# Kernel tuning notes

Measured on AMD Instinct MI355X. Metric: run time of the kernel, lower is better.

The kernel has to match this reference:

```python
import jax, jax.numpy as jnp
import numpy as np
from jax import lax

G = 4  # feature groups in Group_Linear / adjacency
PAD1, PAD2 = 4, 3  # (kern-1)//2 for kern 9 and 7 ('same' time padding)


def _norm_adj(adj):
    # adj: [G, N, N]; add self-loops then symmetric degree normalization
    N = adj.shape[-1]
    adj = adj + jnp.eye(N, dtype=adj.dtype)
    d = jnp.clip(jnp.sum(adj, axis=-1), 1.0, None) ** -0.5
    return d[..., :, None] * adj * d[..., None, :]


def _gcn(x, adj, W, b):
    # DenseGCNConv2d: x [B,C,N,F], adj [G,N,N], W [G,Cout,Cin], b [Cout]
    B, C, N, F = x.shape
    a = _norm_adj(adj)
    xg = x.reshape(B, C, N, G, F // G).transpose(0, 1, 3, 2, 4)  # [B,C,G,N,Fg]
    h = jnp.einsum('goc,bcgnf->bognf', W, xg)                    # grouped 1x1 conv
    out = jnp.einsum('gnm,bogmf->bognf', a, h)                   # adjacency matmul
    Cout = W.shape[1]
    out = out.transpose(0, 1, 3, 2, 4).reshape(B, Cout, N, F)    # regroup features
    return out + b[None, :, None, None]


def _tpool(x, adj, tw, tb, rp, pad):
    # Dense_TimeDiffPool2d: conv over node dim. x [B,C,N,F] -> [B,N,C,F] as NCHW,
    # kernel tw [N', N, 1, k] as OIHW.
    xt = x.transpose(0, 2, 1, 3)
    out = lax.conv_general_dilated(xt, tw, (1, 1), [(0, 0), (pad, pad)],
                                   dimension_numbers=('NCHW', 'OIHW', 'NCHW'))
    out = out + tb[None, :, None, None]
    out = out.transpose(0, 2, 1, 3)                              # [B,C,N',F]
    s = jnp.einsum('pnik,kj->pn', tw, rp)                        # [N',N] assignment
    out_adj = jnp.einsum('pn,gnm,qm->gpq', s, adj, s)            # pooled adjacency
    return out, out_adj


def _forward(x, adj, W1, b1, tw1, tb1, rp1, W2, b2, tw2, tb2, rp2, Wout, bout):
    h = _gcn(x, adj, W1, b1)
    h, a = _tpool(h, adj, tw1, tb1, rp1, PAD1)
    h = jax.nn.relu(h)
    h = _gcn(h, a, W2, b2)
    h, a = _tpool(h, a, tw2, tb2, rp2, PAD2)
    h = jax.nn.relu(h)
    feat = jnp.mean(h, axis=(-1, -2))                            # global pool [B,C]
    return feat @ Wout.T + bout


def setup_inputs():
    key = jax.random.key(0)
    ks = jax.random.split(key, 10)
    B, Cin, Chid, N, F = 16, 1, 32, 128, 512
    N1, N2 = 64, 32
    k1, k2 = 9, 7
    num_classes = 10
    return {
        'x':    jax.random.normal(ks[0], (B, Cin, N, F), jnp.float32),
        'adj':  jax.random.uniform(ks[1], (G, N, N), jnp.float32),
        'W1':   jax.random.normal(ks[2], (G, Chid, Cin), jnp.float32) * 0.5,
        'b1':   jnp.zeros((Chid,), jnp.float32),
        'tw1':  jax.random.normal(ks[3], (N1, N, 1, k1), jnp.float32) * (1.0 / np.sqrt(N * k1)),
        'tb1':  jnp.zeros((N1,), jnp.float32),
        'rp1':  jax.random.normal(ks[4], (k1, 1), jnp.float32),
        'W2':   jax.random.normal(ks[5], (G, Chid, Chid), jnp.float32) * (1.0 / np.sqrt(Chid)),
        'b2':   jnp.zeros((Chid,), jnp.float32),
        'tw2':  jax.random.normal(ks[6], (N2, N1, 1, k2), jnp.float32) * (1.0 / np.sqrt(N1 * k2)),
        'tb2':  jnp.zeros((N2,), jnp.float32),
        'rp2':  jax.random.normal(ks[7], (k2, 1), jnp.float32),
        'Wout': jax.random.normal(ks[8], (num_classes, Chid), jnp.float32) * (1.0 / np.sqrt(Chid)),
        'bout': jnp.zeros((num_classes,), jnp.float32),
    }


def reference(x, adj, W1, b1, tw1, tb1, rp1, W2, b2, tw2, tb2, rp2, Wout, bout):
    return _forward(x, adj, W1, b1, tw1, tb1, rp1, W2, b2, tw2, tb2, rp2, Wout, bout)
```

## Files before the change

### kernel.cpp

```cpp
#include <hip/hip_runtime.h>
#include <math.h>

#define OFF_D1   0
#define OFF_S1   512
#define OFF_T1   8704
#define OFF_TWB  9280
#define OFF_T    16448
#define OFF_A2   49216
#define OFF_A2H  65600
#define OFF_A2L  73792
#define OFF_PART 81984
#define OFF_AN1  82496
#define OFF_C1H  148032
#define OFF_C1L  295488
#define OFF_XTH  442944
#define OFF_XTL  967232
#define OFF_A    1491520
#define OFF_B    9880128
#define OFF_Z    18268736

typedef short bf16x8 __attribute__((ext_vector_type(8)));
typedef short short4v __attribute__((ext_vector_type(4)));
typedef float f32x4 __attribute__((ext_vector_type(4)));

static __device__ __forceinline__ unsigned short f2bf(float x) {
  union { float f; unsigned u; } v; v.f = x;
  unsigned r = v.u + 0x7FFF + ((v.u >> 16) & 1);
  return (unsigned short)(r >> 16);
}
static __device__ __forceinline__ float bf2f(unsigned short h) {
  union { unsigned u; float f; } v; v.u = ((unsigned)h) << 16;
  return v.f;
}

__global__ __launch_bounds__(256) void prep1_kernel(const float* __restrict__ adj,
    const float* __restrict__ tw1, const float* __restrict__ rp1,
    const float* __restrict__ tw2, const float* __restrict__ x,
    float* __restrict__ ws) {
  int t = threadIdx.x;
  if (blockIdx.x < 93) {
    int idx = blockIdx.x * 256 + t;
    if (idx < 512) {
      int g = idx >> 7, n = idx & 127;
      const float* row = adj + (g * 128 + n) * 128;
      float s = 1.0f;
      for (int m = 0; m < 128; ++m) s += row[m];
      ws[OFF_D1 + idx] = 1.0f / sqrtf(fmaxf(s, 1.0f));
    } else if (idx < 8704) {
      int r = idx - 512; int p = r >> 7, n = r & 127;
      const float* tp = tw1 + (p * 128 + n) * 9;
      float s = 0.f;
#pragma unroll
      for (int k = 0; k < 9; ++k) s += tp[k] * rp1[k];
      ws[OFF_S1 + r] = s;
    } else if (idx < 9280) {
      int r = idx - 8704; int p = r / 9, k = r - p * 9;
      float s = 0.f;
      for (int n = 0; n < 128; ++n) s += tw1[(p * 128 + n) * 9 + k];
      ws[OFF_T1 + r] = s;
    } else if (idx < 23616) {
      int r = idx - 9280;
      int q = r / 448, rem = r - q * 448;
      int k = rem >> 6, n = rem & 63;
      ((unsigned short*)(ws + OFF_TWB))[r] = f2bf(tw2[(q * 64 + n) * 7 + k]);
    }
  } else {
    __shared__ float XP[128 * 129];
    int i = blockIdx.x - 93;
    int b = i >> 2, g = i & 3;
#pragma unroll
    for (int ii = 0; ii < 16; ++ii) {
      int e = ii * 256 + t;
      int f4 = e & 31, m = e >> 5;
      float4 v = *(const float4*)&x[(size_t)(b * 128 + m) * 512 + g * 128 + f4 * 4];
      XP[m * 129 + f4 * 4 + 0] = v.x;
      XP[m * 129 + f4 * 4 + 1] = v.y;
      XP[m * 129 + f4 * 4 + 2] = v.z;
      XP[m * 129 + f4 * 4 + 3] = v.w;
    }
    __syncthreads();
    unsigned short* XH = (unsigned short*)(ws + OFF_XTH) + (size_t)(b * 4 + g) * 16384;
    unsigned short* XL = (unsigned short*)(ws + OFF_XTL) + (size_t)(b * 4 + g) * 16384;
#pragma unroll
    for (int ii = 0; ii < 8; ++ii) {
      int e = ii * 256 + t;
      int f = e >> 4, m8 = e & 15;
      unsigned short hs[8], ls[8];
#pragma unroll
      for (int j = 0; j < 8; ++j) {
        float v = XP[(m8 * 8 + j) * 129 + f];
        unsigned short h = f2bf(v);
        hs[j] = h;
        ls[j] = f2bf(v - bf2f(h));
      }
      *(uint4*)&XH[f * 128 + m8 * 8] = *(uint4*)hs;
      *(uint4*)&XL[f * 128 + m8 * 8] = *(uint4*)ls;
    }
  }
}

__global__ __launch_bounds__(256) void prep2_kernel(const float* __restrict__ adj,
                                                    float* __restrict__ ws) {
  int t = threadIdx.x;
  if (blockIdx.x < 256) {
    int idx = blockIdx.x * 256 + t;
    int g = idx >> 14, n = (idx >> 7) & 127, m = idx & 127;
    float v = adj[idx] + (n == m ? 1.0f : 0.0f);
    ws[OFF_AN1 + idx] = ws[OFF_D1 + g * 128 + n] * ws[OFF_D1 + g * 128 + m] * v;
  } else {
    int idx = (blockIdx.x - 256) * 256 + t;
    int g = idx >> 13, n = (idx >> 6) & 127, q = idx & 63;
    const float* row = adj + (g * 128 + n) * 128;
    const float* s1 = ws + OFF_S1 + q * 128;
    float s = 0.f;
    for (int m = 0; m < 128; ++m) s += row[m] * s1[m];
    ws[OFF_T + idx] = s;
  }
}

__global__ __launch_bounds__(256) void prep3_kernel(const float* __restrict__ tw1,
                                                    float* __restrict__ ws) {
  int t = threadIdx.x;
  if (blockIdx.x < 64) {
    int g = blockIdx.x & 3, pt = blockIdx.x >> 2;
    int pp = t >> 6, q = t & 63;
    int p = pt * 4 + pp;
    const float* s1 = ws + OFF_S1 + p * 128;
    const float* tg = ws + OFF_T + g * 8192;
    float s = 0.f;
#pragma unroll 4
    for (int n = 0; n < 128; ++n) s += s1[n] * tg[n * 64 + q];
    ws[OFF_A2 + g * 4096 + p * 64 + q] = s;
  } else {
    int i = blockIdx.x - 64;
    int g = i / 288, rb = i - g * 288;
    int r = rb * 2 + (t >> 7), m = t & 127;
    int p = r / 9, k = r - p * 9;
    const float* an = ws + OFF_AN1 + g * 16384;
    float s = 0.f;
#pragma unroll 4
    for (int n = 0; n < 128; ++n)
      s += tw1[(p * 128 + n) * 9 + k] * an[n * 128 + m];
    unsigned short hi = f2bf(s);
    float lo = s - bf2f(hi);
    ((unsigned short*)(ws + OFF_C1H))[((size_t)g * 576 + r) * 128 + m] = hi;
    ((unsigned short*)(ws + OFF_C1L))[((size_t)g * 576 + r) * 128 + m] = f2bf(lo);
  }
}

__global__ __launch_bounds__(256) void prep4_kernel(float* __restrict__ ws) {
  __shared__ float ap[4096];
  __shared__ float d2[64];
  int g = blockIdx.x, t = threadIdx.x;
  for (int i = t; i < 4096; i += 256) ap[i] = ws[OFF_A2 + g * 4096 + i];
  __syncthreads();
  if (t < 64) {
    float s = 1.0f;
    for (int q = 0; q < 64; ++q) s += ap[t * 64 + q];
    d2[t] = 1.0f / sqrtf(fmaxf(s, 1.0f));
  }
  __syncthreads();
  for (int i = t; i < 4096; i += 256) {
    int p = i >> 6, q = i & 63;
    float fullv = d2[p] * d2[q] * (ap[i] + (p == q ? 1.0f : 0.0f));
    unsigned short hi = f2bf(fullv);
    float lo = fullv - bf2f(hi);
    ((unsigned short*)(ws + OFF_A2H))[g * 4096 + i] = hi;
    ((unsigned short*)(ws + OFF_A2L))[g * 4096 + i] = f2bf(lo);
  }
}

__global__ __launch_bounds__(512) void kz_mfma(float* __restrict__ ws) {
  __shared__ __align__(16) unsigned char smH[32768];
  __shared__ __align__(16) unsigned char smL[32768];
  int b = blockIdx.x, rt = blockIdx.y, g = blockIdx.z, t = threadIdx.x;
  const uint4* XH = (const uint4*)((const unsigned short*)(ws + OFF_XTH) +
                                   (size_t)(b * 4 + g) * 16384);
  const uint4* XL = (const uint4*)((const unsigned short*)(ws + OFF_XTL) +
                                   (size_t)(b * 4 + g) * 16384);
#pragma unroll
  for (int i = 0; i < 4; ++i) {
    int e = i * 512 + t;
    int f = e >> 4, s = e & 15;
    int slot = s ^ (f & 7);
    *(uint4*)(smH + f * 256 + slot * 16) = XH[e];
    *(uint4*)(smL + f * 256 + slot * 16) = XL[e];
  }
  int w = t >> 6, l = t & 63, ll = l & 15, lhi = l >> 4;
  int wm = w & 3, wn = w >> 2;
  const unsigned short* c1h = (const unsigned short*)(ws + OFF_C1H) +
                              ((size_t)g * 576 + rt * 64 + wm * 16 + ll) * 128;
  const unsigned short* c1l = (const unsigned short*)(ws + OFF_C1L) +
                              ((size_t)g * 576 + rt * 64 + wm * 16 + ll) * 128;
  bf16x8 Ah[4], Al[4];
#pragma unroll
  for (int ks = 0; ks < 4; ++ks) {
    Ah[ks] = *(const bf16x8*)(c1h + ks * 32 + lhi * 8);
    Al[ks] = *(const bf16x8*)(c1l + ks * 32 + lhi * 8);
  }
  __syncthreads();
  float* zb = ws + OFF_Z + ((size_t)b * 576 + rt * 64 + wm * 16) * 512 + g * 128 + wn * 64;
#pragma unroll
  for (int Nt = 0; Nt < 4; ++Nt) {
    int f = wn * 64 + Nt * 16 + ll;
    bf16x8 Bh[4], Bl[4];
#pragma unroll
    for (int ks = 0; ks < 4; ++ks) {
      int slot = (ks * 4 + lhi) ^ (f & 7);
      Bh[ks] = *(const bf16x8*)(smH + f * 256 + slot * 16);
      Bl[ks] = *(const bf16x8*)(smL + f * 256 + slot * 16);
    }
    f32x4 acc = {0.f, 0.f, 0.f, 0.f};
#pragma unroll
    for (int ks = 0; ks < 4; ++ks) {
      acc = __builtin_amdgcn_mfma_f32_16x16x32_bf16(Ah[ks], Bh[ks], acc, 0, 0, 0);
      acc = __builtin_amdgcn_mfma_f32_16x16x32_bf16(Ah[ks], Bl[ks], acc, 0, 0, 0);
      acc = __builtin_amdgcn_mfma_f32_16x16x32_bf16(Al[ks], Bh[ks], acc, 0, 0, 0);
    }
#pragma unroll
    for (int i = 0; i < 4; ++i)
      zb[(lhi * 4 + i) * 512 + Nt * 16 + ll] = acc[i];
  }
}

__global__ __launch_bounds__(256) void k45m(const float* __restrict__ W1,
    const float* __restrict__ b1, const float* __restrict__ tb1,
    const float* __restrict__ W2, float* __restrict__ ws) {
  __shared__ float W1s[128];
  __shared__ float b1s[32];
  __shared__ float T1s[9];
  __shared__ __align__(16) unsigned short X2s[256 * 40];
  int b = blockIdx.x, p = blockIdx.y, t = threadIdx.x;
  if (t < 128) W1s[t] = W1[t];
  else if (t < 160) b1s[t - 128] = b1[t - 128];
  else if (t < 169) T1s[t - 160] = ws[OFF_T1 + p * 9 + (t - 160)];
  float tb = tb1[p];
  __syncthreads();
  const float* z = ws + OFF_Z + (size_t)b * 294912 + (size_t)p * 4608;
  unsigned short* vb = (unsigned short*)(ws + OFF_A);
  int w = t >> 6, l = t & 63, ll = l & 15, lhi = l >> 4;
  for (int pass = 0; pass < 2; ++pass) {
    int f = pass * 256 + t;
    float zv[9]; int gk[9];
    float tsum = 0.f;
#pragma unroll
    for (int k = 0; k < 9; ++k) {
      int fp = f + k - 4;
      bool val = (fp >= 0 && fp < 512);
      zv[k] = val ? z[k * 512 + fp] : 0.0f;
      gk[k] = val ? (fp >> 7) : 0;
      tsum += val ? T1s[k] : 0.0f;
    }
    float acc[32];
#pragma unroll
    for (int c = 0; c < 32; ++c) acc[c] = b1s[c] * tsum + tb;
#pragma unroll
    for (int k = 0; k < 9; ++k) {
      const float4* Wc = (const float4*)&W1s[gk[k] * 32];
      float zk = zv[k];
#pragma unroll
      for (int c4 = 0; c4 < 8; ++c4) {
        float4 wv = Wc[c4];
        acc[c4 * 4 + 0] += wv.x * zk;
        acc[c4 * 4 + 1] += wv.y * zk;
        acc[c4 * 4 + 2] += wv.z * zk;
        acc[c4 * 4 + 3] += wv.w * zk;
      }
    }
    __syncthreads();
#pragma unroll
    for (int grp = 0; grp < 4; ++grp) {
      unsigned short hs[8];
#pragma unroll
      for (int j = 0; j < 8; ++j) hs[j] = f2bf(fmaxf(acc[grp * 8 + j], 0.0f));
      *(uint4*)&X2s[t * 40 + grp * 8] = *(uint4*)hs;
    }
    __syncthreads();
    int g = pass * 2 + (w >> 1);
    const float* W2g = W2 + g * 1024;
    bf16x8 Ah[2], Al[2];
#pragma unroll
    for (int Mt = 0; Mt < 2; ++Mt) {
      const float* wp = W2g + (Mt * 16 + ll) * 32 + lhi * 8;
      float wv[8];
      *(float4*)&wv[0] = *(const float4*)wp;
      *(float4*)&wv[4] = *(const float4*)(wp + 4);
      unsigned short hh[8], lw[8];
#pragma unroll
      for (int j = 0; j < 8; ++j) {
        unsigned short h = f2bf(wv[j]);
        hh[j] = h;
        lw[j] = f2bf(wv[j] - bf2f(h));
      }
      Ah[Mt] = *(bf16x8*)hh;
      Al[Mt] = *(bf16x8*)lw;
    }
#pragma unroll
    for (int Nt = 0; Nt < 4; ++Nt) {
      int frow = w * 64 + Nt * 16 + ll;
      bf16x8 Bf = *(const bf16x8*)&X2s[frow * 40 + lhi * 8];
      f32x4 accv[2] = {{0.f, 0.f, 0.f, 0.f}, {0.f, 0.f, 0.f, 0.f}};
#pragma unroll
      for (int Mt = 0; Mt < 2; ++Mt) {
        accv[Mt] = __builtin_amdgcn_mfma_f32_16x16x32_bf16(Ah[Mt], Bf, accv[Mt], 0, 0, 0);
        accv[Mt] = __builtin_amdgcn_mfma_f32_16x16x32_bf16(Al[Mt], Bf, accv[Mt], 0, 0, 0);
      }
      int fglob = pass * 256 + frow;
#pragma unroll
      for (int Mt = 0; Mt < 2; ++Mt)
#pragma unroll
        for (int i = 0; i < 4; ++i) {
          int o = Mt * 16 + lhi * 4 + i;
          vb[((size_t)(b * 32 + o) * 64 + p) * 512 + fglob] = f2bf(accv[Mt][i]);
        }
    }
    __syncthreads();
  }
}

__global__ __launch_bounds__(256) void k5b_h2(const float* __restrict__ b2,
                                              float* __restrict__ ws) {
  __shared__ __align__(16) unsigned short vT[128 * 64];
  int b = blockIdx.x, o = blockIdx.y, g = blockIdx.z, t = threadIdx.x;
  const unsigned short* vbp = (const unsigned short*)(ws + OFF_A) +
                              (size_t)(b * 32 + o) * 32768;
  const uint4* vb4 = (const uint4*)vbp;
  unsigned char* vTw = (unsigned char*)vT;
  for (int i = t; i < 1024; i += 256) {
    int p = i >> 4, u = i & 15;
    uint4 val = vb4[p * 64 + g * 16 + u];
    const unsigned short* hv = (const unsigned short*)&val;
#pragma unroll
    for (int e = 0; e < 8; ++e) {
      int fl = u * 8 + e;
      int addr = fl * 128 + ((p * 2) ^ ((((fl & 7) ^ (fl >> 3)) & 7) << 4));
      *(unsigned short*)(vTw + addr) = hv[e];
    }
  }
  int w = t >> 6, l = t & 63, ll = l & 15, lhi = l >> 4;
  const unsigned short* a2h = (const unsigned short*)(ws + OFF_A2H) + g * 4096;
  const unsigned short* a2l = (const unsigned short*)(ws + OFF_A2L) + g * 4096;
  bf16x8 Ah[4][2], Al[4][2];
#pragma unroll
  for (int Mt = 0; Mt < 4; ++Mt)
#pragma unroll
    for (int ks = 0; ks < 2; ++ks) {
      int idx = (Mt * 16 + ll) * 64 + ks * 32 + lhi * 8;
      Ah[Mt][ks] = *(const bf16x8*)(a2h + idx);
      Al[Mt][ks] = *(const bf16x8*)(a2l + idx);
    }
  float bias = b2[o];
  __syncthreads();
  unsigned short* h2T = (unsigned short*)(ws + OFF_B) + (size_t)(b * 32 + o) * 32768;
  const unsigned char* vTr = (const unsigned char*)vT;
#pragma unroll
  for (int fi = 0; fi < 2; ++fi) {
    int fgl = w * 2 + fi;
    int fl = fgl * 16 + ll;
    int swz = (((fl & 7) ^ (fl >> 3)) & 7) << 4;
    bf16x8 Bf[2];
#pragma unroll
    for (int ks = 0; ks < 2; ++ks)
      Bf[ks] = *(const bf16x8*)(vTr + fl * 128 + ((ks * 64 + lhi * 16) ^ swz));
#pragma unroll
    for (int Mt = 0; Mt < 4; ++Mt) {
      f32x4 acc = {0.f, 0.f, 0.f, 0.f};
      acc = __builtin_amdgcn_mfma_f32_16x16x32_bf16(Ah[Mt][0], Bf[0], acc, 0, 0, 0);
      acc = __builtin_amdgcn_mfma_f32_16x16x32_bf16(Al[Mt][0], Bf[0], acc, 0, 0, 0);
      acc = __builtin_amdgcn_mfma_f32_16x16x32_bf16(Ah[Mt][1], Bf[1], acc, 0, 0, 0);
      acc = __builtin_amdgcn_mfma_f32_16x16x32_bf16(Al[Mt][1], Bf[1], acc, 0, 0, 0);
      int f = g * 128 + fgl * 16 + ll;
      int n0 = Mt * 16 + lhi * 4;
      unsigned short hs[4];
#pragma unroll
      for (int i2 = 0; i2 < 4; ++i2) hs[i2] = f2bf(acc[i2] + bias);
      *(short4v*)(h2T + f * 64 + n0) = *(short4v*)hs;
    }
  }
}

#define L_TWB 66304
#define L_RED 95488
__global__ __launch_bounds__(512) void k6_conv2(const float* __restrict__ tb2,
                                                float* __restrict__ ws) {
  __shared__ __align__(16) unsigned char sm[95520];
  int b = blockIdx.x, c = blockIdx.y, t = threadIdx.x;
  const uint4* h2T4 = (const uint4*)((const unsigned short*)(ws + OFF_B) +
                                     (size_t)(b * 32 + c) * 32768);
  for (int ci = t; ci < 4144; ci += 512) {
    int r = ci >> 3, slot = ci & 7;
    int f = r - 3;
    uint4 val = make_uint4(0u, 0u, 0u, 0u);
    if (f >= 0 && f < 512) val = h2T4[f * 8 + slot];
    *(uint4*)(sm + r * 128 + ((slot ^ (r & 7)) << 4)) = val;
  }
  const uint4* twg = (const uint4*)(ws + OFF_TWB);
  for (int ci = t; ci < 1792; ci += 512) {
    int q = ci / 56, rem = ci - q * 56;
    *(uint4*)(sm + L_TWB + q * 912 + rem * 16) = twg[ci];
  }
  __syncthreads();
  int w = t >> 6, l = t & 63;
  int ll = l & 15, lhi = l >> 4;
  bf16x8 A[2][14];
#pragma unroll
  for (int Mt = 0; Mt < 2; ++Mt)
#pragma unroll
    for (int ks = 0; ks < 14; ++ks) {
      int q = Mt * 16 + ll;
      A[Mt][ks] = *(const bf16x8*)(sm + L_TWB + q * 912 + (ks >> 1) * 128 +
                                   (ks & 1) * 64 + lhi * 16);
    }
  f32x4 zero = {0.f, 0.f, 0.f, 0.f};
  f32x4 acc[2][4];
#pragma unroll
  for (int Mt = 0; Mt < 2; ++Mt)
#pragma unroll
    for (int Nt = 0; Nt < 4; ++Nt) acc[Mt][Nt] = zero;
  int rbase = w * 64 + ll;
#pragma unroll
  for (int ks = 0; ks < 14; ++ks) {
    int rb = rbase + (ks >> 1);
    int x = (((ks & 1) * 4 + lhi) ^ (rb & 7)) << 4;
#pragma unroll
    for (int Nt = 0; Nt < 4; ++Nt) {
      bf16x8 Bf = *(const bf16x8*)(sm + (rb + Nt * 16) * 128 + x);
      acc[0][Nt] = __builtin_amdgcn_mfma_f32_16x16x32_bf16(A[0][ks], Bf, acc[0][Nt], 0, 0, 0);
      acc[1][Nt] = __builtin_amdgcn_mfma_f32_16x16x32_bf16(A[1][ks], Bf, acc[1][Nt], 0, 0, 0);
    }
  }
  float tbv[8];
#pragma unroll
  for (int Mt = 0; Mt < 2; ++Mt)
#pragma unroll
    for (int i = 0; i < 4; ++i) tbv[Mt * 4 + i] = tb2[Mt * 16 + lhi * 4 + i];
  float s = 0.f;
#pragma unroll
  for (int Mt = 0; Mt < 2; ++Mt)
#pragma unroll
    for (int Nt = 0; Nt < 4; ++Nt)
#pragma unroll
      for (int i = 0; i < 4; ++i)
        s += fmaxf(acc[Mt][Nt][i] + tbv[Mt * 4 + i], 0.0f);
#pragma unroll
  for (int off = 32; off > 0; off >>= 1) s += __shfl_down(s, off, 64);
  float* red = (float*)(sm + L_RED);
  if (l == 0) red[w] = s;
  __syncthreads();
  if (t == 0) {
    float tot = 0.f;
    for (int i = 0; i < 8; ++i) tot += red[i];
    ws[OFF_PART + b * 32 + c] = tot;
  }
}

__global__ __launch_bounds__(256) void k7_final(const float* __restrict__ Wout,
    const float* __restrict__ bout, const float* __restrict__ ws, float* __restrict__ out) {
  __shared__ float feat[512];
  int t = threadIdx.x;
  for (int i = t; i < 512; i += 256)
    feat[i] = ws[OFF_PART + i] * (1.0f / 16384.0f);
  __syncthreads();
  if (t < 160) {
    int bb = t / 10, j = t - bb * 10;
    float acc = bout[j];
    for (int c = 0; c < 32; ++c) acc += feat[bb * 32 + c] * Wout[j * 32 + c];
    out[t] = acc;
  }
}

extern "C" void kernel_launch(void* const* d_in, const int* in_sizes, int n_in,
                              void* d_out, int out_size, void* d_ws, size_t ws_size,
                              hipStream_t stream) {
  const float* x    = (const float*)d_in[0];
  const float* adj  = (const float*)d_in[1];
  const float* W1   = (const float*)d_in[2];
  const float* b1   = (const float*)d_in[3];
  const float* tw1  = (const float*)d_in[4];
  const float* tb1  = (const float*)d_in[5];
  const float* rp1  = (const float*)d_in[6];
  const float* W2   = (const float*)d_in[7];
  const float* b2   = (const float*)d_in[8];
  const float* tw2  = (const float*)d_in[9];
  const float* tb2  = (const float*)d_in[10];
  const float* Wout = (const float*)d_in[12];
  const float* bout = (const float*)d_in[13];
  float* out = (float*)d_out;
  float* ws = (float*)d_ws;

  prep1_kernel<<<157, 256, 0, stream>>>(adj, tw1, rp1, tw2, x, ws);
  prep2_kernel<<<384, 256, 0, stream>>>(adj, ws);
  prep3_kernel<<<1216, 256, 0, stream>>>(tw1, ws);
  prep4_kernel<<<4, 256, 0, stream>>>(ws);
  kz_mfma     <<<dim3(16, 9, 4), 512, 0, stream>>>(ws);
  k45m        <<<dim3(16, 64), 256, 0, stream>>>(W1, b1, tb1, W2, ws);
  k5b_h2      <<<dim3(16, 32, 4), 256, 0, stream>>>(b2, ws);
  k6_conv2    <<<dim3(16, 32), 512, 0, stream>>>(tb2, ws);
  k7_final    <<<1, 256, 0, stream>>>(Wout, bout, ws, out);
}
```

Before: 116.1 us.

## Fuse second GCN adjacency matmul into conv2 kernel via shared-memory staging

Result: slower. 119.0 us (+2.5%).

```diff
diff --git a/kernel.cpp b/kernel.cpp
--- a/kernel.cpp
+++ b/kernel.cpp
@@ -16,7 +16,6 @@
 #define OFF_XTH  442944
 #define OFF_XTL  967232
 #define OFF_A    1491520
-#define OFF_B    9880128
 #define OFF_Z    18268736
 
 typedef short bf16x8 __attribute__((ext_vector_type(8)));
@@ -318,50 +317,62 @@
   }
 }
 
-__global__ __launch_bounds__(256) void k5b_h2(const float* __restrict__ b2,
-                                              float* __restrict__ ws) {
-  __shared__ __align__(16) unsigned short vT[128 * 64];
-  int b = blockIdx.x, o = blockIdx.y, g = blockIdx.z, t = threadIdx.x;
+#define L_VT  66304
+#define L_TWB 82688
+#define L_RED 111872
+__global__ __launch_bounds__(512) void k56_fused(const float* __restrict__ b2,
+    const float* __restrict__ tb2, float* __restrict__ ws) {
+  __shared__ __align__(16) unsigned char sm[111904];
+  int b = blockIdx.x, o = blockIdx.y, t = threadIdx.x;
+  int w = t >> 6, l = t & 63, ll = l & 15, lhi = l >> 4;
+  if (t < 48) {
+    const short zr[6] = {0, 1, 2, 515, 516, 517};
+    int row = zr[t >> 3], slot = t & 7;
+    *(uint4*)(sm + row * 128 + slot * 16) = make_uint4(0u, 0u, 0u, 0u);
+  }
+  const uint4* twg = (const uint4*)(ws + OFF_TWB);
+  for (int ci = t; ci < 1792; ci += 512) {
+    int q = ci / 56, rem = ci - q * 56;
+    *(uint4*)(sm + L_TWB + q * 912 + rem * 16) = twg[ci];
+  }
   const unsigned short* vbp = (const unsigned short*)(ws + OFF_A) +
                               (size_t)(b * 32 + o) * 32768;
   const uint4* vb4 = (const uint4*)vbp;
-  unsigned char* vTw = (unsigned char*)vT;
-  for (int i = t; i < 1024; i += 256) {
-    int p = i >> 4, u = i & 15;
-    uint4 val = vb4[p * 64 + g * 16 + u];
-    const unsigned short* hv = (const unsigned short*)&val;
-#pragma unroll
-    for (int e = 0; e < 8; ++e) {
-      int fl = u * 8 + e;
-      int addr = fl * 128 + ((p * 2) ^ ((((fl & 7) ^ (fl >> 3)) & 7) << 4));
-      *(unsigned short*)(vTw + addr) = hv[e];
-    }
-  }
-  int w = t >> 6, l = t & 63, ll = l & 15, lhi = l >> 4;
-  const unsigned short* a2h = (const unsigned short*)(ws + OFF_A2H) + g * 4096;
-  const unsigned short* a2l = (const unsigned short*)(ws + OFF_A2L) + g * 4096;
-  bf16x8 Ah[4][2], Al[4][2];
-#pragma unroll
-  for (int Mt = 0; Mt < 4; ++Mt)
-#pragma unroll
-    for (int ks = 0; ks < 2; ++ks) {
-      int idx = (Mt * 16 + ll) * 64 + ks * 32 + lhi * 8;
-      Ah[Mt][ks] = *(const bf16x8*)(a2h + idx);
-      Al[Mt][ks] = *(const bf16x8*)(a2l + idx);
-    }
   float bias = b2[o];
-  __syncthreads();
-  unsigned short* h2T = (unsigned short*)(ws + OFF_B) + (size_t)(b * 32 + o) * 32768;
-  const unsigned char* vTr = (const unsigned char*)vT;
-#pragma unroll
-  for (int fi = 0; fi < 2; ++fi) {
-    int fgl = w * 2 + fi;
+  for (int g = 0; g < 4; ++g) {
+    __syncthreads();
+    for (int i = t; i < 1024; i += 512) {
+      int p = i >> 4, u = i & 15;
+      uint4 val = vb4[p * 64 + g * 16 + u];
+      const unsigned short* hv = (const unsigned short*)&val;
+#pragma unroll
+      for (int e = 0; e < 8; ++e) {
+        int fl = u * 8 + e;
+        int addr = L_VT + fl * 128 + ((p * 2) ^ ((((fl & 7) ^ (fl >> 3)) & 7) << 4));
+        *(unsigned short*)(sm + addr) = hv[e];
+      }
+    }
+    const unsigned short* a2h = (const unsigned short*)(ws + OFF_A2H) + g * 4096;
+    const unsigned short* a2l = (const unsigned short*)(ws + OFF_A2L) + g * 4096;
+    bf16x8 Ah[4][2], Al[4][2];
+#pragma unroll
+    for (int Mt = 0; Mt < 4; ++Mt)
+#pragma unroll
+      for (int ks = 0; ks < 2; ++ks) {
+        int idx = (Mt * 16 + ll) * 64 + ks * 32 + lhi * 8;
+        Ah[Mt][ks] = *(const bf16x8*)(a2h + idx);
+        Al[Mt][ks] = *(const bf16x8*)(a2l + idx);
+      }
+    __syncthreads();
+    int fgl = w;
     int fl = fgl * 16 + ll;
     int swz = (((fl & 7) ^ (fl >> 3)) & 7) << 4;
     bf16x8 Bf[2];
 #pragma unroll
     for (int ks = 0; ks < 2; ++ks)
-      Bf[ks] = *(const bf16x8*)(vTr + fl * 128 + ((ks * 64 + lhi * 16) ^ swz));
+      Bf[ks] = *(const bf16x8*)(sm + L_VT + fl * 128 + ((ks * 64 + lhi * 16) ^ swz));
+    int f = g * 128 + fgl * 16 + ll;
+    int r = f + 3;
 #pragma unroll
     for (int Mt = 0; Mt < 4; ++Mt) {
       f32x4 acc = {0.f, 0.f, 0.f, 0.f};
@@ -369,39 +380,15 @@
       acc = __builtin_amdgcn_mfma_f32_16x16x32_bf16(Al[Mt][0], Bf[0], acc, 0, 0, 0);
       acc = __builtin_amdgcn_mfma_f32_16x16x32_bf16(Ah[Mt][1], Bf[1], acc, 0, 0, 0);
       acc = __builtin_amdgcn_mfma_f32_16x16x32_bf16(Al[Mt][1], Bf[1], acc, 0, 0, 0);
-      int f = g * 128 + fgl * 16 + ll;
       int n0 = Mt * 16 + lhi * 4;
       unsigned short hs[4];
 #pragma unroll
       for (int i2 = 0; i2 < 4; ++i2) hs[i2] = f2bf(acc[i2] + bias);
-      *(short4v*)(h2T + f * 64 + n0) = *(short4v*)hs;
-    }
-  }
-}
-
-#define L_TWB 66304
-#define L_RED 95488
-__global__ __launch_bounds__(512) void k6_conv2(const float* __restrict__ tb2,
-                                                float* __restrict__ ws) {
-  __shared__ __align__(16) unsigned char sm[95520];
-  int b = blockIdx.x, c = blockIdx.y, t = threadIdx.x;
-  const uint4* h2T4 = (const uint4*)((const unsigned short*)(ws + OFF_B) +
-                                     (size_t)(b * 32 + c) * 32768);
-  for (int ci = t; ci < 4144; ci += 512) {
-    int r = ci >> 3, slot = ci & 7;
-    int f = r - 3;
-    uint4 val = make_uint4(0u, 0u, 0u, 0u);
-    if (f >= 0 && f < 512) val = h2T4[f * 8 + slot];
-    *(uint4*)(sm + r * 128 + ((slot ^ (r & 7)) << 4)) = val;
-  }
-  const uint4* twg = (const uint4*)(ws + OFF_TWB);
-  for (int ci = t; ci < 1792; ci += 512) {
-    int q = ci / 56, rem = ci - q * 56;
-    *(uint4*)(sm + L_TWB + q * 912 + rem * 16) = twg[ci];
-  }
-  __syncthreads();
-  int w = t >> 6, l = t & 63;
-  int ll = l & 15, lhi = l >> 4;
+      int dest = r * 128 + ((((n0 >> 3) ^ (r & 7)) << 4)) + (n0 & 7) * 2;
+      *(short4v*)(sm + dest) = *(short4v*)hs;
+    }
+  }
+  __syncthreads();
   bf16x8 A[2][14];
 #pragma unroll
   for (int Mt = 0; Mt < 2; ++Mt)
@@ -450,7 +437,7 @@
   if (t == 0) {
     float tot = 0.f;
     for (int i = 0; i < 8; ++i) tot += red[i];
-    ws[OFF_PART + b * 32 + c] = tot;
+    ws[OFF_PART + b * 32 + o] = tot;
   }
 }
 
@@ -494,7 +481,6 @@
   prep4_kernel<<<4, 256, 0, stream>>>(ws);
   kz_mfma     <<<dim3(16, 9, 4), 512, 0, stream>>>(ws);
   k45m        <<<dim3(16, 64), 256, 0, stream>>>(W1, b1, tb1, W2, ws);
-  k5b_h2      <<<dim3(16, 32, 4), 256, 0, stream>>>(b2, ws);
-  k6_conv2    <<<dim3(16, 32), 512, 0, stream>>>(tb2, ws);
+  k56_fused   <<<dim3(16, 32), 512, 0, stream>>>(b2, tb2, ws);
   k7_final    <<<1, 256, 0, stream>>>(Wout, bout, ws, out);
 }
```

## Merge prep kernels into one cooperative kernel and fuse final FC into conv2

Applied to the files above, without the earlier changes.

After: 302.3 us. 2.6x slower.

```diff
diff --git a/kernel.cpp b/kernel.cpp
--- a/kernel.cpp
+++ b/kernel.cpp
@@ -1,5 +1,8 @@
 #include <hip/hip_runtime.h>
+#include <hip/hip_cooperative_groups.h>
 #include <math.h>
+
+namespace cg = cooperative_groups;
 
 #define OFF_D1   0
 #define OFF_S1   512
@@ -18,6 +21,7 @@
 #define OFF_A    1491520
 #define OFF_B    9880128
 #define OFF_Z    18268736
+#define OFF_CTR  22987328
 
 typedef short bf16x8 __attribute__((ext_vector_type(8)));
 typedef short short4v __attribute__((ext_vector_type(4)));
@@ -33,13 +37,16 @@
   return v.f;
 }
 
-__global__ __launch_bounds__(256) void prep1_kernel(const float* __restrict__ adj,
+__global__ __launch_bounds__(256) void coop_prep(const float* __restrict__ adj,
     const float* __restrict__ tw1, const float* __restrict__ rp1,
     const float* __restrict__ tw2, const float* __restrict__ x,
     float* __restrict__ ws) {
-  int t = threadIdx.x;
-  if (blockIdx.x < 93) {
-    int idx = blockIdx.x * 256 + t;
+  __shared__ __align__(16) unsigned char smb[16640];
+  int t = threadIdx.x, bid = blockIdx.x;
+  cg::grid_group grid = cg::this_grid();
+  if (bid == 0 && t == 0) ((unsigned*)(ws + OFF_CTR))[0] = 0u;
+  if (bid < 93) {
+    int idx = bid * 256 + t;
     if (idx < 512) {
       int g = idx >> 7, n = idx & 127;
       const float* row = adj + (g * 128 + n) * 128;
@@ -64,51 +71,50 @@
       int k = rem >> 6, n = rem & 63;
       ((unsigned short*)(ws + OFF_TWB))[r] = f2bf(tw2[(q * 64 + n) * 7 + k]);
     }
-  } else {
-    __shared__ float XP[128 * 129];
-    int i = blockIdx.x - 93;
+  } else if (bid < 157) {
+    float* XP2 = (float*)smb;
+    int i = bid - 93;
     int b = i >> 2, g = i & 3;
-#pragma unroll
-    for (int ii = 0; ii < 16; ++ii) {
-      int e = ii * 256 + t;
-      int f4 = e & 31, m = e >> 5;
-      float4 v = *(const float4*)&x[(size_t)(b * 128 + m) * 512 + g * 128 + f4 * 4];
-      XP[m * 129 + f4 * 4 + 0] = v.x;
-      XP[m * 129 + f4 * 4 + 1] = v.y;
-      XP[m * 129 + f4 * 4 + 2] = v.z;
-      XP[m * 129 + f4 * 4 + 3] = v.w;
-    }
-    __syncthreads();
     unsigned short* XH = (unsigned short*)(ws + OFF_XTH) + (size_t)(b * 4 + g) * 16384;
     unsigned short* XL = (unsigned short*)(ws + OFF_XTL) + (size_t)(b * 4 + g) * 16384;
-#pragma unroll
-    for (int ii = 0; ii < 8; ++ii) {
-      int e = ii * 256 + t;
-      int f = e >> 4, m8 = e & 15;
-      unsigned short hs[8], ls[8];
-#pragma unroll
-      for (int j = 0; j < 8; ++j) {
-        float v = XP[(m8 * 8 + j) * 129 + f];
-        unsigned short h = f2bf(v);
-        hs[j] = h;
-        ls[j] = f2bf(v - bf2f(h));
+    for (int mi = 0; mi < 4; ++mi) {
+      __syncthreads();
+#pragma unroll
+      for (int ii = 0; ii < 4; ++ii) {
+        int e = ii * 256 + t;
+        int r = e >> 5, f4 = e & 31;
+        float4 v = *(const float4*)&x[(size_t)(b * 128 + mi * 32 + r) * 512 + g * 128 + f4 * 4];
+        XP2[r * 129 + f4 * 4 + 0] = v.x;
+        XP2[r * 129 + f4 * 4 + 1] = v.y;
+        XP2[r * 129 + f4 * 4 + 2] = v.z;
+        XP2[r * 129 + f4 * 4 + 3] = v.w;
       }
-      *(uint4*)&XH[f * 128 + m8 * 8] = *(uint4*)hs;
-      *(uint4*)&XL[f * 128 + m8 * 8] = *(uint4*)ls;
-    }
-  }
-}
-
-__global__ __launch_bounds__(256) void prep2_kernel(const float* __restrict__ adj,
-                                                    float* __restrict__ ws) {
-  int t = threadIdx.x;
-  if (blockIdx.x < 256) {
-    int idx = blockIdx.x * 256 + t;
+      __syncthreads();
+#pragma unroll
+      for (int ii = 0; ii < 2; ++ii) {
+        int e = ii * 256 + t;
+        int f = e >> 2, m8 = e & 3;
+        unsigned short hs[8], ls[8];
+#pragma unroll
+        for (int j = 0; j < 8; ++j) {
+          float v = XP2[(m8 * 8 + j) * 129 + f];
+          unsigned short h = f2bf(v);
+          hs[j] = h;
+          ls[j] = f2bf(v - bf2f(h));
+        }
+        *(uint4*)&XH[f * 128 + mi * 32 + m8 * 8] = *(uint4*)hs;
+        *(uint4*)&XL[f * 128 + mi * 32 + m8 * 8] = *(uint4*)ls;
+      }
+    }
+  }
+  grid.sync();
+  if (bid < 256) {
+    int idx = bid * 256 + t;
     int g = idx >> 14, n = (idx >> 7) & 127, m = idx & 127;
     float v = adj[idx] + (n == m ? 1.0f : 0.0f);
     ws[OFF_AN1 + idx] = ws[OFF_D1 + g * 128 + n] * ws[OFF_D1 + g * 128 + m] * v;
-  } else {
-    int idx = (blockIdx.x - 256) * 256 + t;
+  } else if (bid < 384) {
+    int idx = (bid - 256) * 256 + t;
     int g = idx >> 13, n = (idx >> 6) & 127, q = idx & 63;
     const float* row = adj + (g * 128 + n) * 128;
     const float* s1 = ws + OFF_S1 + q * 128;
@@ -116,57 +122,55 @@
     for (int m = 0; m < 128; ++m) s += row[m] * s1[m];
     ws[OFF_T + idx] = s;
   }
-}
-
-__global__ __launch_bounds__(256) void prep3_kernel(const float* __restrict__ tw1,
-                                                    float* __restrict__ ws) {
-  int t = threadIdx.x;
-  if (blockIdx.x < 64) {
-    int g = blockIdx.x & 3, pt = blockIdx.x >> 2;
-    int pp = t >> 6, q = t & 63;
-    int p = pt * 4 + pp;
-    const float* s1 = ws + OFF_S1 + p * 128;
-    const float* tg = ws + OFF_T + g * 8192;
-    float s = 0.f;
+  grid.sync();
+  for (int u = bid; u < 1216; u += 512) {
+    if (u < 64) {
+      int g = u & 3, pt = u >> 2;
+      int pp = t >> 6, q = t & 63;
+      int p = pt * 4 + pp;
+      const float* s1 = ws + OFF_S1 + p * 128;
+      const float* tg = ws + OFF_T + g * 8192;
+      float s = 0.f;
 #pragma unroll 4
-    for (int n = 0; n < 128; ++n) s += s1[n] * tg[n * 64 + q];
-    ws[OFF_A2 + g * 4096 + p * 64 + q] = s;
-  } else {
-    int i = blockIdx.x - 64;
-    int g = i / 288, rb = i - g * 288;
-    int r = rb * 2 + (t >> 7), m = t & 127;
-    int p = r / 9, k = r - p * 9;
-    const float* an = ws + OFF_AN1 + g * 16384;
-    float s = 0.f;
+      for (int n = 0; n < 128; ++n) s += s1[n] * tg[n * 64 + q];
+      ws[OFF_A2 + g * 4096 + p * 64 + q] = s;
+    } else {
+      int i = u - 64;
+      int g = i / 288, rb = i - g * 288;
+      int r = rb * 2 + (t >> 7), m = t & 127;
+      int p = r / 9, k = r - p * 9;
+      const float* an = ws + OFF_AN1 + g * 16384;
+      float s = 0.f;
 #pragma unroll 4
-    for (int n = 0; n < 128; ++n)
-      s += tw1[(p * 128 + n) * 9 + k] * an[n * 128 + m];
-    unsigned short hi = f2bf(s);
-    float lo = s - bf2f(hi);
-    ((unsigned short*)(ws + OFF_C1H))[((size_t)g * 576 + r) * 128 + m] = hi;
-    ((unsigned short*)(ws + OFF_C1L))[((size_t)g * 576 + r) * 128 + m] = f2bf(lo);
-  }
-}
-
-__global__ __launch_bounds__(256) void prep4_kernel(float* __restrict__ ws) {
-  __shared__ float ap[4096];
-  __shared__ float d2[64];
-  int g = blockIdx.x, t = threadIdx.x;
-  for (int i = t; i < 4096; i += 256) ap[i] = ws[OFF_A2 + g * 4096 + i];
-  __syncthreads();
-  if (t < 64) {
-    float s = 1.0f;
-    for (int q = 0; q < 64; ++q) s += ap[t * 64 + q];
-    d2[t] = 1.0f / sqrtf(fmaxf(s, 1.0f));
-  }
-  __syncthreads();
-  for (int i = t; i < 4096; i += 256) {
-    int p = i >> 6, q = i & 63;
-    float fullv = d2[p] * d2[q] * (ap[i] + (p == q ? 1.0f : 0.0f));
-    unsigned short hi = f2bf(fullv);
-    float lo = fullv - bf2f(hi);
-    ((unsigned short*)(ws + OFF_A2H))[g * 4096 + i] = hi;
-    ((unsigned short*)(ws + OFF_A2L))[g * 4096 + i] = f2bf(lo);
+      for (int n = 0; n < 128; ++n)
+        s += tw1[(p * 128 + n) * 9 + k] * an[n * 128 + m];
+      unsigned short hi = f2bf(s);
+      float lo = s - bf2f(hi);
+      ((unsigned short*)(ws + OFF_C1H))[((size_t)g * 576 + r) * 128 + m] = hi;
+      ((unsigned short*)(ws + OFF_C1L))[((size_t)g * 576 + r) * 128 + m] = f2bf(lo);
+    }
+  }
+  grid.sync();
+  if (bid < 4) {
+    float* ap = (float*)smb;
+    float* d2 = (float*)(smb + 16384);
+    int g = bid;
+    for (int i = t; i < 4096; i += 256) ap[i] = ws[OFF_A2 + g * 4096 + i];
+    __syncthreads();
+    if (t < 64) {
+      float s = 1.0f;
+      for (int q = 0; q < 64; ++q) s += ap[t * 64 + q];
+      d2[t] = 1.0f / sqrtf(fmaxf(s, 1.0f));
+    }
+    __syncthreads();
+    for (int i = t; i < 4096; i += 256) {
+      int p = i >> 6, q = i & 63;
+      float fullv = d2[p] * d2[q] * (ap[i] + (p == q ? 1.0f : 0.0f));
+      unsigned short hi = f2bf(fullv);
+      float lo = fullv - bf2f(hi);
+      ((unsigned short*)(ws + OFF_A2H))[g * 4096 + i] = hi;
+      ((unsigned short*)(ws + OFF_A2L))[g * 4096 + i] = f2bf(lo);
+    }
   }
 }
 
@@ -381,9 +385,11 @@
 
 #define L_TWB 66304
 #define L_RED 95488
+#define L_FLAG 95520
 __global__ __launch_bounds__(512) void k6_conv2(const float* __restrict__ tb2,
-                                                float* __restrict__ ws) {
-  __shared__ __align__(16) unsigned char sm[95520];
+    const float* __restrict__ Wout, const float* __restrict__ bout,
+    float* __restrict__ ws, float* __restrict__ out) {
+  __shared__ __align__(16) unsigned char sm[95524];
   int b = blockIdx.x, c = blockIdx.y, t = threadIdx.x;
   const uint4* h2T4 = (const uint4*)((const unsigned short*)(ws + OFF_B) +
                                      (size_t)(b * 32 + c) * 32768);
@@ -450,22 +456,23 @@
   if (t == 0) {
     float tot = 0.f;
     for (int i = 0; i < 8; ++i) tot += red[i];
-    ws[OFF_PART + b * 32 + c] = tot;
-  }
-}
-
-__global__ __launch_bounds__(256) void k7_final(const float* __restrict__ Wout,
-    const float* __restrict__ bout, const float* __restrict__ ws, float* __restrict__ out) {
-  __shared__ float feat[512];
-  int t = threadIdx.x;
-  for (int i = t; i < 512; i += 256)
-    feat[i] = ws[OFF_PART + i] * (1.0f / 16384.0f);
+    atomicExch(&ws[OFF_PART + b * 32 + c], tot);
+    __threadfence();
+    unsigned old = atomicAdd((unsigned*)(ws + OFF_CTR), 1u);
+    *(volatile unsigned*)(sm + L_FLAG) = (old == 511u) ? 1u : 0u;
+  }
   __syncthreads();
-  if (t < 160) {
-    int bb = t / 10, j = t - bb * 10;
-    float acc = bout[j];
-    for (int c = 0; c < 32; ++c) acc += feat[bb * 32 + c] * Wout[j * 32 + c];
-    out[t] = acc;
+  if (*(volatile unsigned*)(sm + L_FLAG)) {
+    __threadfence();
+    float* feat = (float*)sm;
+    if (t < 512) feat[t] = ws[OFF_PART + t] * (1.0f / 16384.0f);
+    __syncthreads();
+    if (t < 160) {
+      int bb = t / 10, j = t - bb * 10;
+      float accf = bout[j];
+      for (int c2 = 0; c2 < 32; ++c2) accf += feat[bb * 32 + c2] * Wout[j * 32 + c2];
+      out[t] = accf;
+    }
   }
 }
 
@@ -488,13 +495,11 @@
   float* out = (float*)d_out;
   float* ws = (float*)d_ws;
 
-  prep1_kernel<<<157, 256, 0, stream>>>(adj, tw1, rp1, tw2, x, ws);
-  prep2_kernel<<<384, 256, 0, stream>>>(adj, ws);
-  prep3_kernel<<<1216, 256, 0, stream>>>(tw1, ws);
-  prep4_kernel<<<4, 256, 0, stream>>>(ws);
-  kz_mfma     <<<dim3(16, 9, 4), 512, 0, stream>>>(ws);
-  k45m        <<<dim3(16, 64), 256, 0, stream>>>(W1, b1, tb1, W2, ws);
-  k5b_h2      <<<dim3(16, 32, 4), 256, 0, stream>>>(b2, ws);
-  k6_conv2    <<<dim3(16, 32), 512, 0, stream>>>(tb2, ws);
-  k7_final    <<<1, 256, 0, stream>>>(Wout, bout, ws, out);
-}
+  void* cargs[] = {(void*)&adj, (void*)&tw1, (void*)&rp1, (void*)&tw2,
+                   (void*)&x, (void*)&ws};
+  hipLaunchCooperativeKernel((void*)coop_prep, dim3(512), dim3(256), cargs, 0u, stream);
+  kz_mfma <<<dim3(16, 9, 4), 512, 0, stream>>>(ws);
+  k45m    <<<dim3(16, 64), 256, 0, stream>>>(W1, b1, tb1, W2, ws);
+  k5b_h2  <<<dim3(16, 32, 4), 256, 0, stream>>>(b2, ws);
+  k6_conv2<<<dim3(16, 32), 512, 0, stream>>>(tb2, Wout, bout, ws, out);
+}
```
